# Kernel tuning notes

Hardware: AMD Instinct MI355X
Metric: run time of the kernel (lower is better)

## Reference

```python
import jax, jax.numpy as jnp
import numpy as np

HEAD_COUNT = 16  # original code scales by head_count ** -0.5 (not head_size)


def setup_inputs() -> dict:
    key = jax.random.key(0)
    k1, k2, k3, k4 = jax.random.split(key, 4)
    B, T, C, H = 4, 4096, 1024, 64
    x = jax.random.normal(k1, (B, T, C), dtype=jnp.float32)
    # nn.Linear(C, H, bias=False) weights, stored as (C, H) so projection is x @ W
    Wq = jax.random.normal(k2, (C, H), dtype=jnp.float32) * (C ** -0.5)
    Wk = jax.random.normal(k3, (C, H), dtype=jnp.float32) * (C ** -0.5)
    Wv = jax.random.normal(k4, (C, H), dtype=jnp.float32) * (C ** -0.5)
    return {"x": x, "Wq": Wq, "Wk": Wk, "Wv": Wv}


def reference(x, Wq, Wk, Wv):
    B, T, C = x.shape
    q = jnp.einsum('btc,ch->bth', x, Wq)  # [B,T,H]
    k = jnp.einsum('btc,ch->bth', x, Wk)
    v = jnp.einsum('btc,ch->bth', x, Wv)
    scale = HEAD_COUNT ** (-0.5)
    scores = jnp.einsum('bth,bsh->bts', q, k) * scale  # [B,T,T]
    causal = jnp.tril(jnp.ones((T, T), dtype=bool))
    scores = jnp.where(causal, scores, -jnp.inf)
    weights = jax.nn.softmax(scores, axis=-1)
    # dropout disabled (eval / rate 0) for deterministic reference
    out = jnp.einsum('bts,bsh->bth', weights, v)  # [B,T,H]
    return out
```

## Files before the change

### kernel.cpp

```cpp
#include <hip/hip_runtime.h>
#include <hip/hip_bf16.h>


typedef __attribute__((ext_vector_type(8))) short short8_t;
typedef __attribute__((ext_vector_type(4))) float f32x4;
typedef __attribute__((ext_vector_type(16))) float f32x16;

#define MFMA16(a, b, c) __builtin_amdgcn_mfma_f32_16x16x32_bf16((a), (b), (c), 0, 0, 0)
#define MFMA32(a, b, c) __builtin_amdgcn_mfma_f32_32x32x16_bf16((a), (b), (c), 0, 0, 0)

__device__ __forceinline__ unsigned short f2bf(float f) {
  union { float f; unsigned int u; } v; v.f = f;
  unsigned int u = v.u;
  u += 0x7FFFu + ((u >> 16) & 1u);
  return (unsigned short)(u >> 16);
}
__device__ __forceinline__ float bf2f(unsigned short h) {
  union { unsigned int u; float f; } v; v.u = ((unsigned int)h) << 16;
  return v.f;
}

__device__ __forceinline__ size_t vtidx(int b, int t, int h) {
  return ((((((size_t)b * 128 + (t >> 5)) * 2 + (h >> 5)) * 2 + ((t >> 4) & 1)) * 2
           + ((t >> 3) & 1)) * 32 + (h & 31)) * 8 + (t & 7);
}

__global__ __launch_bounds__(192) void wprep(
    const float* __restrict__ Wq, const float* __restrict__ Wk,
    const float* __restrict__ Wv,
    unsigned short* __restrict__ wth, unsigned short* __restrict__ wtl)
{
  const int n  = threadIdx.x;
  const int kb = blockIdx.x;
  const float* W = (n < 64) ? Wq : (n < 128) ? Wk : Wv;
  const int cc = n & 63;
  union { unsigned short u[8]; short8_t s; } uh, ul;
#pragma unroll
  for (int j = 0; j < 8; ++j) {
    float f = W[(size_t)(kb * 8 + j) * 64 + cc];
    unsigned short h = f2bf(f);
    uh.u[j] = h;
    ul.u[j] = f2bf(f - bf2f(h));
  }
  *reinterpret_cast<short8_t*>(wth + (size_t)n * 1024 + kb * 8) = uh.s;
  *reinterpret_cast<short8_t*>(wtl + (size_t)n * 1024 + kb * 8) = ul.s;
}

__global__ __launch_bounds__(256) void qkv_proj(
    const float* __restrict__ x,
    const unsigned short* __restrict__ wth, const unsigned short* __restrict__ wtl,
    unsigned short* __restrict__ qh, unsigned short* __restrict__ ql,
    unsigned short* __restrict__ kh, unsigned short* __restrict__ kl,
    unsigned short* __restrict__ vth, unsigned short* __restrict__ vtl)
{
  const int tid  = threadIdx.x;
  const int wave = tid >> 6;
  const int lane = tid & 63;
  const int g    = lane >> 4;
  const int c    = lane & 15;
  const int m0   = blockIdx.x * 32;

  f32x4 acc[2][3];
#pragma unroll
  for (int m = 0; m < 2; ++m)
#pragma unroll
    for (int nn = 0; nn < 3; ++nn) acc[m][nn] = (f32x4){0.f, 0.f, 0.f, 0.f};

  for (int k0 = 0; k0 < 1024; k0 += 32) {
    short8_t a_h[2], a_l[2];
#pragma unroll
    for (int m = 0; m < 2; ++m) {
      const float* xp = x + (size_t)(m0 + m * 16 + c) * 1024 + k0 + g * 8;
      const float4 f0 = *reinterpret_cast<const float4*>(xp);
      const float4 f1 = *reinterpret_cast<const float4*>(xp + 4);
      union { unsigned short u[8]; short8_t s; } uh, ul;
#pragma unroll
      for (int j = 0; j < 4; ++j) {
        float fa = ((const float*)&f0)[j];
        unsigned short ha = f2bf(fa);
        uh.u[j] = ha; ul.u[j] = f2bf(fa - bf2f(ha));
        float fb = ((const float*)&f1)[j];
        unsigned short hb = f2bf(fb);
        uh.u[4 + j] = hb; ul.u[4 + j] = f2bf(fb - bf2f(hb));
      }
      a_h[m] = uh.s; a_l[m] = ul.s;
    }
#pragma unroll
    for (int nn = 0; nn < 3; ++nn) {
      const int nt = wave * 3 + nn;
      const size_t bo = (size_t)(nt * 16 + c) * 1024 + k0 + g * 8;
      const short8_t b_h = *reinterpret_cast<const short8_t*>(wth + bo);
      const short8_t b_l = *reinterpret_cast<const short8_t*>(wtl + bo);
#pragma unroll
      for (int m = 0; m < 2; ++m) {
        acc[m][nn] = MFMA16(a_h[m], b_h, acc[m][nn]);
        acc[m][nn] = MFMA16(a_h[m], b_l, acc[m][nn]);
        acc[m][nn] = MFMA16(a_l[m], b_h, acc[m][nn]);
      }
    }
  }

#pragma unroll
  for (int m = 0; m < 2; ++m) {
#pragma unroll
    for (int nn = 0; nn < 3; ++nn) {
      const int nt  = wave * 3 + nn;
      const int col = nt * 16 + c;
      const int mat = col >> 6;
      const int cm  = col & 63;
#pragma unroll
      for (int r = 0; r < 4; ++r) {
        float f = acc[m][nn][r];
        int row = m0 + m * 16 + g * 4 + r;
        unsigned short h  = f2bf(f);
        unsigned short lo = f2bf(f - bf2f(h));
        if (mat == 0)      { size_t i = (size_t)row * 64 + cm; qh[i] = h; ql[i] = lo; }
        else if (mat == 1) { size_t i = (size_t)row * 64 + cm; kh[i] = h; kl[i] = lo; }
        else {
          int bb = row >> 12, t = row & 4095;
          size_t i = vtidx(bb, t, cm);
          vth[i] = h; vtl[i] = lo;
        }
      }
    }
  }
}

#define MASKVAL (-3.0e38f)
#define MINIT   (-1.0e30f)

__global__ __launch_bounds__(256, 2) void attn(
    const unsigned short* __restrict__ qh, const unsigned short* __restrict__ ql,
    const unsigned short* __restrict__ kh, const unsigned short* __restrict__ kl,
    const unsigned short* __restrict__ vth, const unsigned short* __restrict__ vtl,
    float* __restrict__ Opart, float* __restrict__ MLpart)
{
  __shared__ alignas(16) unsigned char smem[70656];

  const int tid = threadIdx.x;
  const int ws  = tid >> 6;
  const int l   = tid & 63;
  const int h5  = l >> 5;
  const int l31 = l & 31;

  const int bidb = blockIdx.x;
  const int bb   = bidb / 160;
  const int s    = bidb % 160;
  int jt, slice, nsl;
  if (s < 16)      { jt = s;                         slice = 0;                nsl = 1; }
  else if (s < 48) { int i = s - 16; jt = 16 + (i >> 1); slice = i & 1;        nsl = 2; }
  else if (s < 96) { int i = s - 48; jt = 32 + i / 3;    slice = i - 3 * (jt - 32); nsl = 3; }
  else             { int i = s - 96; jt = 48 + (i >> 2); slice = i & 3;        nsl = 4; }
  const int t0    = jt * 64;
  const int total = 2 * (jt + 1);
  const int k0t   = (slice * total) / nsl;
  const int k1t   = ((slice + 1) * total) / nsl;

  const float CE = 0.36067376022224085f;

  short8_t qf_h[2][4], qf_l[2][4];
#pragma unroll
  for (int qt = 0; qt < 2; ++qt)
#pragma unroll
    for (int cc = 0; cc < 4; ++cc) {
      size_t off = ((size_t)(bb * 4096 + t0 + qt * 32 + l31)) * 64 + cc * 16 + h5 * 8;
      qf_h[qt][cc] = *reinterpret_cast<const short8_t*>(qh + off);
      qf_l[qt][cc] = *reinterpret_cast<const short8_t*>(ql + off);
    }

  f32x16 ot[2][2];
#pragma unroll
  for (int a = 0; a < 2; ++a)
#pragma unroll
    for (int b2 = 0; b2 < 2; ++b2)
#pragma unroll
      for (int r = 0; r < 16; ++r) ot[a][b2][r] = 0.f;
  float mreg[2] = {MINIT, MINIT};
  float lreg[2] = {0.f, 0.f};

  for (int kti = k0t + ws; kti < k1t; kti += 4) {
    const int s0 = kti * 32;

    short8_t kf_h[4], kf_l[4];
    const size_t krow = ((size_t)(bb * 4096 + s0 + l31)) * 64 + h5 * 8;
#pragma unroll
    for (int cc = 0; cc < 4; ++cc) {
      kf_h[cc] = *reinterpret_cast<const short8_t*>(kh + krow + cc * 16);
      kf_l[cc] = *reinterpret_cast<const short8_t*>(kl + krow + cc * 16);
    }

    short8_t pfh[2][2], pfl[2][2];

#pragma unroll
    for (int qt = 0; qt < 2; ++qt) {
      if (s0 > t0 + qt * 32 + 31) {
        union { int d[4]; short8_t s8; } z;
        z.d[0] = z.d[1] = z.d[2] = z.d[3] = 0;
        pfh[qt][0] = z.s8; pfh[qt][1] = z.s8;
        pfl[qt][0] = z.s8; pfl[qt][1] = z.s8;
        continue;
      }

      f32x16 st;
#pragma unroll
      for (int r = 0; r < 16; ++r) st[r] = 0.f;
#pragma unroll
      for (int cc = 0; cc < 4; ++cc) {
        st = MFMA32(kf_h[cc], qf_h[qt][cc], st);
        st = MFMA32(kf_h[cc], qf_l[qt][cc], st);
        st = MFMA32(kf_l[cc], qf_h[qt][cc], st);
      }

      if (s0 + 31 > t0 + qt * 32) {
        int qg = t0 + qt * 32 + l31;
#pragma unroll
        for (int r = 0; r < 16; ++r) {
          int keyg = s0 + (r & 3) + 8 * (r >> 2) + 4 * h5;
          if (keyg > qg) st[r] = MASKVAL;
        }
      }

      float pm = st[0];
#pragma unroll
      for (int r = 1; r < 16; ++r) pm = fmaxf(pm, st[r]);
      pm = fmaxf(pm, __shfl_xor(pm, 32));
      float mnew = fmaxf(mreg[qt], pm);
      float fs = __builtin_amdgcn_exp2f((mreg[qt] - mnew) * CE);
      mreg[qt] = mnew;
      lreg[qt] *= fs;
#pragma unroll
      for (int ht = 0; ht < 2; ++ht) ot[ht][qt] *= fs;

      float p[16]; float rs = 0.f;
#pragma unroll
      for (int r = 0; r < 16; ++r) {
        p[r] = __builtin_amdgcn_exp2f((st[r] - mnew) * CE);
        rs += p[r];
      }
      rs += __shfl_xor(rs, 32);
      lreg[qt] += rs;

      int w[8], wl[8], pw[8], pwl[8];
#pragma unroll
      for (int i = 0; i < 8; ++i) {
        unsigned short b0 = f2bf(p[2 * i]), b1 = f2bf(p[2 * i + 1]);
        w[i] = (int)((unsigned)b0 | ((unsigned)b1 << 16));
        float l0 = p[2 * i] - bf2f(b0), l1 = p[2 * i + 1] - bf2f(b1);
        wl[i] = (int)((unsigned)f2bf(l0) | ((unsigned)f2bf(l1) << 16));
      }
#pragma unroll
      for (int i = 0; i < 8; ++i) {
        pw[i]  = __shfl_xor(w[i], 32);
        pwl[i] = __shfl_xor(wl[i], 32);
      }
#pragma unroll
      for (int kc = 0; kc < 2; ++kc) {
        union { int d[4]; short8_t s8; } uh2, ul2;
        uh2.d[0] = h5 ? pw[4 * kc + 2]  : w[4 * kc];
        uh2.d[1] = h5 ? pw[4 * kc + 3]  : w[4 * kc + 1];
        uh2.d[2] = h5 ? w[4 * kc + 2]   : pw[4 * kc];
        uh2.d[3] = h5 ? w[4 * kc + 3]   : pw[4 * kc + 1];
        ul2.d[0] = h5 ? pwl[4 * kc + 2] : wl[4 * kc];
        ul2.d[1] = h5 ? pwl[4 * kc + 3] : wl[4 * kc + 1];
        ul2.d[2] = h5 ? wl[4 * kc + 2]  : pwl[4 * kc];
        ul2.d[3] = h5 ? wl[4 * kc + 3]  : pwl[4 * kc + 1];
        pfh[qt][kc] = uh2.s8;
        pfl[qt][kc] = ul2.s8;
      }
    }

#pragma unroll
    for (int ht = 0; ht < 2; ++ht)
#pragma unroll
      for (int kc = 0; kc < 2; ++kc) {
        const size_t vbase =
            ((size_t)(((bb * 128 + kti) * 2 + ht) * 2 + kc)) * 512 + (size_t)l * 8;
        const short8_t vfh = *reinterpret_cast<const short8_t*>(vth + vbase);
        const short8_t vfl = *reinterpret_cast<const short8_t*>(vtl + vbase);
#pragma unroll
        for (int qt = 0; qt < 2; ++qt) {
          ot[ht][qt] = MFMA32(vfh, pfh[qt][kc], ot[ht][qt]);
          ot[ht][qt] = MFMA32(vfl, pfh[qt][kc], ot[ht][qt]);
          ot[ht][qt] = MFMA32(vfh, pfl[qt][kc], ot[ht][qt]);
        }
      }
  }

  float* OT = (float*)smem;
  float* ML = (float*)(smem + 68608);
#pragma unroll
  for (int ht = 0; ht < 2; ++ht)
#pragma unroll
    for (int qt = 0; qt < 2; ++qt)
#pragma unroll
      for (int r = 0; r < 16; ++r) {
        int hrow = ht * 32 + (r & 3) + 8 * (r >> 2) + 4 * h5;
        int q = qt * 32 + l31;
        OT[(ws * 64 + hrow) * 67 + q] = ot[ht][qt][r];
      }
  if (l < 32) {
#pragma unroll
    for (int qt = 0; qt < 2; ++qt) {
      int q = qt * 32 + l31;
      ML[(ws * 64 + q) * 2]     = mreg[qt];
      ML[(ws * 64 + q) * 2 + 1] = lreg[qt];
    }
  }
  __syncthreads();

  {
    const int h  = tid & 63;
    const int qg = tid >> 6;
#pragma unroll
    for (int i = 0; i < 16; ++i) {
      int q = qg * 16 + i;
      float M = ML[q * 2];
#pragma unroll
      for (int s2 = 1; s2 < 4; ++s2) M = fmaxf(M, ML[(s2 * 64 + q) * 2]);
      float L = 0.f, A = 0.f;
#pragma unroll
      for (int s2 = 0; s2 < 4; ++s2) {
        float wgt = __builtin_amdgcn_exp2f((ML[(s2 * 64 + q) * 2] - M) * CE);
        L += wgt * ML[(s2 * 64 + q) * 2 + 1];
        A += wgt * OT[(s2 * 64 + h) * 67 + q];
      }
      Opart[((size_t)bidb * 64 + q) * 64 + h] = A;
      if (h == 0) MLpart[((size_t)bidb * 64 + q) * 2]     = M;
      if (h == 1) MLpart[((size_t)bidb * 64 + q) * 2 + 1] = L;
    }
  }
}

__global__ __launch_bounds__(256) void attn_merge(
    const float* __restrict__ Opart, const float* __restrict__ MLpart,
    float* __restrict__ out)
{
  const int bid = blockIdx.x;
  const int bb = bid >> 6, jt = bid & 63;
  const int nsl = 1 + (jt >= 16) + (jt >= 32) + (jt >= 48);
  const int off = (jt < 16) ? jt
                : (jt < 32) ? 16 + 2 * (jt - 16)
                : (jt < 48) ? 48 + 3 * (jt - 32)
                :             96 + 4 * (jt - 48);
  const int pid0 = bb * 160 + off;
  const int t = threadIdx.x;
  const int q = t >> 2;
  const int hg = t & 3;
  const float CE = 0.36067376022224085f;

  float M = MLpart[((size_t)pid0 * 64 + q) * 2];
  for (int s2 = 1; s2 < nsl; ++s2)
    M = fmaxf(M, MLpart[((size_t)(pid0 + s2) * 64 + q) * 2]);

  float L = 0.f;
  float a[16];
#pragma unroll
  for (int j = 0; j < 16; ++j) a[j] = 0.f;

  for (int s2 = 0; s2 < nsl; ++s2) {
    size_t mlb = ((size_t)(pid0 + s2) * 64 + q) * 2;
    float w = __builtin_amdgcn_exp2f((MLpart[mlb] - M) * CE);
    L += w * MLpart[mlb + 1];
    const float* op = Opart + ((size_t)(pid0 + s2) * 64 + q) * 64 + hg * 16;
#pragma unroll
    for (int j = 0; j < 4; ++j) {
      float4 v4 = *reinterpret_cast<const float4*>(op + j * 4);
      a[j * 4 + 0] += w * v4.x; a[j * 4 + 1] += w * v4.y;
      a[j * 4 + 2] += w * v4.z; a[j * 4 + 3] += w * v4.w;
    }
  }

  const float inv = 1.f / L;
  float* po = out + ((size_t)bb * 4096 + jt * 64 + q) * 64 + hg * 16;
#pragma unroll
  for (int j = 0; j < 4; ++j) {
    float4 v4 = { a[j * 4] * inv, a[j * 4 + 1] * inv,
                  a[j * 4 + 2] * inv, a[j * 4 + 3] * inv };
    *reinterpret_cast<float4*>(po + j * 4) = v4;
  }
}

extern "C" void kernel_launch(void* const* d_in, const int* in_sizes, int n_in,
                              void* d_out, int out_size, void* d_ws, size_t ws_size,
                              hipStream_t stream) {
  const float* x  = (const float*)d_in[0];
  const float* Wq = (const float*)d_in[1];
  const float* Wk = (const float*)d_in[2];
  const float* Wv = (const float*)d_in[3];
  float* out = (float*)d_out;

  const size_t NE = (size_t)16384 * 64;
  unsigned short* qh  = (unsigned short*)d_ws;
  unsigned short* ql  = qh + NE;
  unsigned short* kh  = ql + NE;
  unsigned short* kl  = kh + NE;
  unsigned short* vth = kl + NE;
  unsigned short* vtl = vth + NE;
  unsigned short* wth = vtl + NE;
  unsigned short* wtl = wth + (size_t)192 * 1024;
  float* Opart  = (float*)(wtl + (size_t)192 * 1024);
  float* MLpart = Opart + (size_t)640 * 64 * 64;

  wprep<<<128, 192, 0, stream>>>(Wq, Wk, Wv, wth, wtl);
  qkv_proj<<<512, 256, 0, stream>>>(x, wth, wtl, qh, ql, kh, kl, vth, vtl);
  attn<<<640, 256, 0, stream>>>(qh, ql, kh, kl, vth, vtl, Opart, MLpart);
  attn_merge<<<256, 256, 0, stream>>>(Opart, MLpart, out);
}
```

Baseline: 237.0 us.

## Double-buffer QKV projection loads, remap attention blocks per XCD, raise MFMA priority

The QKV projection now prefetches the next K-slice of x and the weights into registers while computing the current one, and declares two blocks per SIMD in its launch bounds. The attention kernel remaps block IDs so each XCD handles one batch, which should keep K/V reuse inside one L2. It also hoists the V fragment loads ahead of the PV MFMAs and raises wave priority with s_setprio around MFMA bursts. Costs are higher register pressure in the projection, which may cap occupancy, and one wasted wrap-around prefetch at the end of its loop.

```diff
diff --git a/kernel.cpp b/kernel.cpp
--- a/kernel.cpp
+++ b/kernel.cpp
@@ -46,7 +46,7 @@
   *reinterpret_cast<short8_t*>(wtl + (size_t)n * 1024 + kb * 8) = ul.s;
 }
 
-__global__ __launch_bounds__(256) void qkv_proj(
+__global__ __launch_bounds__(256, 2) void qkv_proj(
     const float* __restrict__ x,
     const unsigned short* __restrict__ wth, const unsigned short* __restrict__ wtl,
     unsigned short* __restrict__ qh, unsigned short* __restrict__ ql,
@@ -60,45 +60,62 @@
   const int c    = lane & 15;
   const int m0   = blockIdx.x * 32;
 
+  const float* xb = x + (size_t)(m0 + c) * 1024 + g * 8;
+  const unsigned short* bhb = wth + (size_t)(wave * 48 + c) * 1024 + g * 8;
+  const unsigned short* blb = wtl + (size_t)(wave * 48 + c) * 1024 + g * 8;
+
   f32x4 acc[2][3];
 #pragma unroll
   for (int m = 0; m < 2; ++m)
 #pragma unroll
     for (int nn = 0; nn < 3; ++nn) acc[m][nn] = (f32x4){0.f, 0.f, 0.f, 0.f};
 
-  for (int k0 = 0; k0 < 1024; k0 += 32) {
-    short8_t a_h[2], a_l[2];
-#pragma unroll
-    for (int m = 0; m < 2; ++m) {
-      const float* xp = x + (size_t)(m0 + m * 16 + c) * 1024 + k0 + g * 8;
-      const float4 f0 = *reinterpret_cast<const float4*>(xp);
-      const float4 f1 = *reinterpret_cast<const float4*>(xp + 4);
-      union { unsigned short u[8]; short8_t s; } uh, ul;
-#pragma unroll
-      for (int j = 0; j < 4; ++j) {
-        float fa = ((const float*)&f0)[j];
-        unsigned short ha = f2bf(fa);
-        uh.u[j] = ha; ul.u[j] = f2bf(fa - bf2f(ha));
-        float fb = ((const float*)&f1)[j];
-        unsigned short hb = f2bf(fb);
-        uh.u[4 + j] = hb; ul.u[4 + j] = f2bf(fb - bf2f(hb));
-      }
-      a_h[m] = uh.s; a_l[m] = ul.s;
-    }
-#pragma unroll
-    for (int nn = 0; nn < 3; ++nn) {
-      const int nt = wave * 3 + nn;
-      const size_t bo = (size_t)(nt * 16 + c) * 1024 + k0 + g * 8;
-      const short8_t b_h = *reinterpret_cast<const short8_t*>(wth + bo);
-      const short8_t b_l = *reinterpret_cast<const short8_t*>(wtl + bo);
-#pragma unroll
-      for (int m = 0; m < 2; ++m) {
-        acc[m][nn] = MFMA16(a_h[m], b_h, acc[m][nn]);
-        acc[m][nn] = MFMA16(a_h[m], b_l, acc[m][nn]);
-        acc[m][nn] = MFMA16(a_l[m], b_h, acc[m][nn]);
-      }
-    }
-  }
+  float4 A0[4], A1[4];
+  short8_t B0h[3], B0l[3], B1h[3], B1l[3];
+
+#define LOADA(buf, kk) do {                                                  \
+    _Pragma("unroll") for (int m_ = 0; m_ < 2; ++m_) {                       \
+      const float* p_ = xb + (size_t)m_ * 16384 + (kk);                      \
+      buf[m_ * 2]     = *reinterpret_cast<const float4*>(p_);                \
+      buf[m_ * 2 + 1] = *reinterpret_cast<const float4*>(p_ + 4);            \
+    } } while (0)
+#define LOADB(bh, bl, kk) do {                                               \
+    _Pragma("unroll") for (int nn_ = 0; nn_ < 3; ++nn_) {                    \
+      const size_t bo_ = (size_t)nn_ * 16384 + (kk);                         \
+      bh[nn_] = *reinterpret_cast<const short8_t*>(bhb + bo_);               \
+      bl[nn_] = *reinterpret_cast<const short8_t*>(blb + bo_);               \
+    } } while (0)
+#define STEP(Abuf, Bh, Bl) do {                                              \
+    short8_t a_h[2], a_l[2];                                                 \
+    _Pragma("unroll") for (int m_ = 0; m_ < 2; ++m_) {                       \
+      union { unsigned short u[8]; short8_t s; } uh_, ul_;                   \
+      _Pragma("unroll") for (int hf_ = 0; hf_ < 2; ++hf_) {                  \
+        const float4 f_ = Abuf[m_ * 2 + hf_];                                \
+        _Pragma("unroll") for (int j_ = 0; j_ < 4; ++j_) {                   \
+          float fv_ = ((const float*)&f_)[j_];                               \
+          unsigned short hh_ = f2bf(fv_);                                    \
+          uh_.u[hf_ * 4 + j_] = hh_;                                         \
+          ul_.u[hf_ * 4 + j_] = f2bf(fv_ - bf2f(hh_));                       \
+        } }                                                                  \
+      a_h[m_] = uh_.s; a_l[m_] = ul_.s; }                                    \
+    _Pragma("unroll") for (int nn_ = 0; nn_ < 3; ++nn_)                      \
+      _Pragma("unroll") for (int m_ = 0; m_ < 2; ++m_) {                     \
+        acc[m_][nn_] = MFMA16(a_h[m_], Bh[nn_], acc[m_][nn_]);               \
+        acc[m_][nn_] = MFMA16(a_h[m_], Bl[nn_], acc[m_][nn_]);               \
+        acc[m_][nn_] = MFMA16(a_l[m_], Bh[nn_], acc[m_][nn_]);               \
+      } } while (0)
+
+  LOADA(A0, 0); LOADB(B0h, B0l, 0);
+  for (int k0 = 0; k0 < 1024; k0 += 64) {
+    LOADA(A1, k0 + 32); LOADB(B1h, B1l, k0 + 32);
+    STEP(A0, B0h, B0l);
+    const int kn = (k0 + 64 < 1024) ? k0 + 64 : 0;
+    LOADA(A0, kn); LOADB(B0h, B0l, kn);
+    STEP(A1, B1h, B1l);
+  }
+#undef LOADA
+#undef LOADB
+#undef STEP
 
 #pragma unroll
   for (int m = 0; m < 2; ++m) {
@@ -143,14 +160,17 @@
   const int h5  = l >> 5;
   const int l31 = l & 31;
 
-  const int bidb = blockIdx.x;
-  const int bb   = bidb / 160;
-  const int s    = bidb % 160;
+  const int bid0 = blockIdx.x;
+  const int xcd  = bid0 & 7;
+  const int bb   = xcd >> 1;
+  const int s    = ((bid0 >> 3) << 1) | (xcd & 1);
+  const int bidb = bb * 160 + s;
+
   int jt, slice, nsl;
-  if (s < 16)      { jt = s;                         slice = 0;                nsl = 1; }
-  else if (s < 48) { int i = s - 16; jt = 16 + (i >> 1); slice = i & 1;        nsl = 2; }
+  if (s < 16)      { jt = s;                             slice = 0;                nsl = 1; }
+  else if (s < 48) { int i = s - 16; jt = 16 + (i >> 1); slice = i & 1;            nsl = 2; }
   else if (s < 96) { int i = s - 48; jt = 32 + i / 3;    slice = i - 3 * (jt - 32); nsl = 3; }
-  else             { int i = s - 96; jt = 48 + (i >> 2); slice = i & 3;        nsl = 4; }
+  else             { int i = s - 96; jt = 48 + (i >> 2); slice = i & 3;            nsl = 4; }
   const int t0    = jt * 64;
   const int total = 2 * (jt + 1);
   const int k0t   = (slice * total) / nsl;
@@ -204,12 +224,14 @@
       f32x16 st;
 #pragma unroll
       for (int r = 0; r < 16; ++r) st[r] = 0.f;
+      __builtin_amdgcn_s_setprio(1);
 #pragma unroll
       for (int cc = 0; cc < 4; ++cc) {
         st = MFMA32(kf_h[cc], qf_h[qt][cc], st);
         st = MFMA32(kf_h[cc], qf_l[qt][cc], st);
         st = MFMA32(kf_l[cc], qf_h[qt][cc], st);
       }
+      __builtin_amdgcn_s_setprio(0);
 
       if (s0 + 31 > t0 + qt * 32) {
         int qg = t0 + qt * 32 + l31;
@@ -269,21 +291,29 @@
       }
     }
 
+    short8_t vfh[2][2], vfl[2][2];
 #pragma unroll
     for (int ht = 0; ht < 2; ++ht)
 #pragma unroll
       for (int kc = 0; kc < 2; ++kc) {
         const size_t vbase =
             ((size_t)(((bb * 128 + kti) * 2 + ht) * 2 + kc)) * 512 + (size_t)l * 8;
-        const short8_t vfh = *reinterpret_cast<const short8_t*>(vth + vbase);
-        const short8_t vfl = *reinterpret_cast<const short8_t*>(vtl + vbase);
+        vfh[ht][kc] = *reinterpret_cast<const short8_t*>(vth + vbase);
+        vfl[ht][kc] = *reinterpret_cast<const short8_t*>(vtl + vbase);
+      }
+
+    __builtin_amdgcn_s_setprio(1);
+#pragma unroll
+    for (int ht = 0; ht < 2; ++ht)
+#pragma unroll
+      for (int kc = 0; kc < 2; ++kc)
 #pragma unroll
         for (int qt = 0; qt < 2; ++qt) {
-          ot[ht][qt] = MFMA32(vfh, pfh[qt][kc], ot[ht][qt]);
-          ot[ht][qt] = MFMA32(vfl, pfh[qt][kc], ot[ht][qt]);
-          ot[ht][qt] = MFMA32(vfh, pfl[qt][kc], ot[ht][qt]);
+          ot[ht][qt] = MFMA32(vfh[ht][kc], pfh[qt][kc], ot[ht][qt]);
+          ot[ht][qt] = MFMA32(vfl[ht][kc], pfh[qt][kc], ot[ht][qt]);
+          ot[ht][qt] = MFMA32(vfh[ht][kc], pfl[qt][kc], ot[ht][qt]);
         }
-      }
+    __builtin_amdgcn_s_setprio(0);
   }
 
   float* OT = (float*)smem;
```

After: 230.0 us. 3.0% less time.
